# Performance work log

Hardware: AMD Instinct MI355X
Metric: run time of the kernel (lower is better)

## Reference

```python
import jax, jax.numpy as jnp
import numpy as np

B, T, D_ENC, D_DEC, D_ATT = 64, 4096, 512, 512, 256


def setup_inputs() -> dict:
    keys = jax.random.split(jax.random.key(0), 8)
    h_enc = jax.random.normal(keys[0], (B, T, D_ENC), dtype=jnp.float32)
    h_dec = jax.random.normal(keys[1], (B, 1, D_DEC), dtype=jnp.float32)
    mask = jax.random.randint(keys[2], (B, T), 0, 2).astype(bool)
    s = 0.02
    Wq_w = jax.random.normal(keys[3], (D_ATT, D_DEC), dtype=jnp.float32) * s
    Wq_b = jnp.zeros((D_ATT,), dtype=jnp.float32)
    Wk_w = jax.random.normal(keys[4], (D_ATT, D_ENC), dtype=jnp.float32) * s
    Wk_b = jnp.zeros((D_ATT,), dtype=jnp.float32)
    v_w = jax.random.normal(keys[5], (1, D_ATT), dtype=jnp.float32) * s
    return {"h_enc": h_enc, "h_dec": h_dec, "Wq_w": Wq_w, "Wq_b": Wq_b,
            "Wk_w": Wk_w, "Wk_b": Wk_b, "v_w": v_w, "mask": mask}


def reference(h_enc, h_dec, Wq_w, Wq_b, Wk_w, Wk_b, v_w, mask):
    # q: [B,1,d_att], k: [B,T,d_att]
    q = jnp.einsum('bqe,ae->bqa', h_dec, Wq_w) + Wq_b
    k = jnp.einsum('bte,ae->bta', h_enc, Wk_w) + Wk_b
    # additive (Bahdanau) score: v^T tanh(q + k) -> [B,T]
    scores = jnp.einsum('bta,a->bt', jnp.tanh(q + k), v_w[0])
    scores = jnp.where(mask, scores, jnp.float32(-1e9))
    w = jax.nn.softmax(scores, axis=1)          # [B,T]
    ctx = jnp.einsum('bt,bte->be', w, h_enc)    # [B,d_enc]
    return ctx, w
```

## Files before the change

### kernel.cpp

```cpp
#include <hip/hip_runtime.h>
#include <math.h>

#define B    64
#define T    4096
#define DENC 512
#define DDEC 512
#define DATT 256

typedef __attribute__((ext_vector_type(8))) short          short8;
typedef __attribute__((ext_vector_type(8))) unsigned short ushort8v;
typedef __attribute__((ext_vector_type(4))) float          f32x4;

__device__ __forceinline__ unsigned short f2bf(float f) {
    union { float f; unsigned u; } v; v.f = f;
    return (unsigned short)((v.u + 0x7fffu + ((v.u >> 16) & 1u)) >> 16);
}

__device__ __forceinline__ unsigned pk2bf(float a, float b) {
    unsigned ua = __float_as_uint(a) + 0x8000u;
    unsigned ub = __float_as_uint(b) + 0x8000u;
    return __builtin_amdgcn_perm(ub, ua, 0x07060302u);
}

__device__ __forceinline__ float bf2f(unsigned short u) {
    return __uint_as_float((unsigned)u << 16);
}

__device__ __forceinline__ float tanh_fast(float x) {
    float e = __expf(2.0f * x);
    return 1.0f - 2.0f / (e + 1.0f);
}

__global__ __launch_bounds__(256) void k_wkconv(const float* __restrict__ Wk_w,
                                                unsigned short* __restrict__ WkB) {
    int i = (blockIdx.x * 256 + threadIdx.x) * 4;
    float4 v = *(const float4*)(Wk_w + i);
    ushort4 o;
    o.x = f2bf(v.x); o.y = f2bf(v.y); o.z = f2bf(v.z); o.w = f2bf(v.w);
    *(ushort4*)(WkB + i) = o;
}

__global__ __launch_bounds__(256) void k_qproj(const float* __restrict__ h_dec,
                                               const float* __restrict__ Wq_w,
                                               const float* __restrict__ Wq_b,
                                               const float* __restrict__ Wk_b,
                                               float* __restrict__ qq) {
    __shared__ float sh[DDEC];
    const int b = blockIdx.x;
    const int tid = threadIdx.x;
    ((float2*)sh)[tid] = ((const float2*)(h_dec + (size_t)b * DDEC))[tid];
    __syncthreads();
    const int a = tid;
    const float4* wr  = (const float4*)(Wq_w + (size_t)a * DDEC);
    const float4* shv = (const float4*)sh;
    float acc = 0.f;
#pragma unroll 4
    for (int i = 0; i < DDEC / 4; ++i) {
        float4 wv = wr[i];
        float4 hv = shv[i];
        acc += wv.x * hv.x + wv.y * hv.y + wv.z * hv.z + wv.w * hv.w;
    }
    qq[b * DATT + a] = acc + Wq_b[a] + Wk_b[a];
}

#define BM 128
#define BK 32

__global__ __launch_bounds__(256, 2) void k_score(const float* __restrict__ h_enc,
                                                  const unsigned short* __restrict__ WkB,
                                                  const float* __restrict__ qq,
                                                  const float* __restrict__ v_w,
                                                  const int* __restrict__ mask,
                                                  unsigned short* __restrict__ hB,
                                                  float* __restrict__ scores) {
    __shared__ short As[BM * BK];
    __shared__ short Bs[DATT * BK];
    __shared__ float sp[2][BM];

    const int tc   = blockIdx.x;
    const int b    = blockIdx.y;
    const int tid  = threadIdx.x;
    const int wv   = tid >> 6;
    const int lane = tid & 63;
    const int ln15 = lane & 15;
    const int qd   = lane >> 4;
    const int wv_t = wv >> 1;
    const int wv_a = wv & 1;
    const int t0   = tc * BM;

    f32x4 acc[4][8];
#pragma unroll
    for (int i = 0; i < 4; ++i)
#pragma unroll
        for (int j = 0; j < 8; ++j) acc[i][j] = (f32x4){0.f, 0.f, 0.f, 0.f};

    const float* Abase = h_enc + ((size_t)b * T + t0) * DENC;
    unsigned short* hBbase = hB + ((size_t)b * T + t0) * DENC;

    for (int k0 = 0; k0 < DENC; k0 += BK) {
#pragma unroll
        for (int it = 0; it < 4; ++it) {
            int idx = (wv * 4 + it) * 64 + lane;
            int r   = idx >> 2;
            int cc  = (idx & 3) ^ ((r >> 1) & 3);
            const unsigned short* gp = WkB + (size_t)r * DENC + k0 + cc * 8;
            short* lp = &Bs[(wv * 4 + it) * 64 * 8];
            __builtin_amdgcn_global_load_lds(
                (const __attribute__((address_space(1))) unsigned int*)gp,
                (__attribute__((address_space(3))) unsigned int*)lp, 16, 0, 0);
        }
#pragma unroll
        for (int it = 0; it < 2; ++it) {
            int idx = it * 256 + tid;
            int r   = idx >> 2;
            int cc  = (idx & 3) ^ ((r >> 1) & 3);
            const float* gp = Abase + (size_t)r * DENC + k0 + cc * 8;
            float4 v0 = *(const float4*)gp;
            float4 v1 = *(const float4*)(gp + 4);
            uint4 pk;
            pk.x = pk2bf(v0.x, v0.y);
            pk.y = pk2bf(v0.z, v0.w);
            pk.z = pk2bf(v1.x, v1.y);
            pk.w = pk2bf(v1.z, v1.w);
            *(uint4*)&As[idx * 8] = pk;
            *(uint4*)(hBbase + (size_t)r * DENC + k0 + cc * 8) = pk;
        }
        __syncthreads();

        short8 af[4], bfr[8];
#pragma unroll
        for (int ti = 0; ti < 4; ++ti) {
            int r = wv_t * 64 + ti * 16 + ln15;
            int s = qd ^ ((r >> 1) & 3);
            af[ti] = *(const short8*)&As[r * 32 + s * 8];
        }
#pragma unroll
        for (int tj = 0; tj < 8; ++tj) {
            int r = wv_a * 128 + tj * 16 + ln15;
            int s = qd ^ ((r >> 1) & 3);
            bfr[tj] = *(const short8*)&Bs[r * 32 + s * 8];
        }
#pragma unroll
        for (int ti = 0; ti < 4; ++ti)
#pragma unroll
            for (int tj = 0; tj < 8; ++tj)
                acc[ti][tj] = __builtin_amdgcn_mfma_f32_16x16x32_bf16(
                    af[ti], bfr[tj], acc[ti][tj], 0, 0, 0);
        __syncthreads();
    }

    float qr[8], vr[8];
#pragma unroll
    for (int tj = 0; tj < 8; ++tj) {
        int a = wv_a * 128 + tj * 16 + ln15;
        qr[tj] = qq[b * DATT + a];
        vr[tj] = v_w[a];
    }
#pragma unroll
    for (int ti = 0; ti < 4; ++ti) {
#pragma unroll
        for (int rg = 0; rg < 4; ++rg) {
            float s = 0.f;
#pragma unroll
            for (int tj = 0; tj < 8; ++tj)
                s += vr[tj] * tanh_fast(qr[tj] + acc[ti][tj][rg]);
            s += __shfl_xor(s, 1, 64);
            s += __shfl_xor(s, 2, 64);
            s += __shfl_xor(s, 4, 64);
            s += __shfl_xor(s, 8, 64);
            if (ln15 == 0)
                sp[wv_a][wv_t * 64 + ti * 16 + qd * 4 + rg] = s;
        }
    }
    __syncthreads();
    if (tid < BM) {
        int t = t0 + tid;
        float s = sp[0][tid] + sp[1][tid];
        bool m = mask[(size_t)b * T + t] != 0;
        scores[(size_t)b * T + t] = m ? s : -1e9f;
    }
}

__global__ __launch_bounds__(256) void k_softmax(float* __restrict__ w) {
    const int b = blockIdx.x;
    const int tid = threadIdx.x;
    const int wid = tid >> 6, lane = tid & 63;
    float* row = w + (size_t)b * T;
    __shared__ float red[4];
    __shared__ float bmax_s, bsum_s;

    float x[T / 256];
#pragma unroll
    for (int i = 0; i < T / 256; ++i) x[i] = row[tid + i * 256];

    float lmax = -INFINITY;
#pragma unroll
    for (int i = 0; i < T / 256; ++i) lmax = fmaxf(lmax, x[i]);
#pragma unroll
    for (int off = 32; off >= 1; off >>= 1) lmax = fmaxf(lmax, __shfl_xor(lmax, off, 64));
    if (lane == 0) red[wid] = lmax;
    __syncthreads();
    if (tid == 0) bmax_s = fmaxf(fmaxf(red[0], red[1]), fmaxf(red[2], red[3]));
    __syncthreads();
    const float bmax = bmax_s;

    float lsum = 0.f;
#pragma unroll
    for (int i = 0; i < T / 256; ++i) { x[i] = __expf(x[i] - bmax); lsum += x[i]; }
#pragma unroll
    for (int off = 32; off >= 1; off >>= 1) lsum += __shfl_xor(lsum, off, 64);
    if (lane == 0) red[wid] = lsum;
    __syncthreads();
    if (tid == 0) bsum_s = red[0] + red[1] + red[2] + red[3];
    __syncthreads();
    const float inv = 1.f / bsum_s;
#pragma unroll
    for (int i = 0; i < T / 256; ++i) row[tid + i * 256] = x[i] * inv;
}

#define TCH 512
__global__ __launch_bounds__(256) void k_ctx(const unsigned short* __restrict__ hB,
                                             const float* __restrict__ w,
                                             float* __restrict__ ctx) {
    const int b   = blockIdx.y;
    const int t0  = blockIdx.x * TCH;
    const int tid = threadIdx.x;
    const int lane = tid & 63, wv = tid >> 6;
    const int e8 = lane * 8;
    __shared__ float ws[TCH];
    __shared__ float red[3][DENC];

    ((float2*)ws)[tid] = ((const float2*)(w + (size_t)b * T + t0))[tid];
    __syncthreads();

    const unsigned short* hp = hB + ((size_t)(b * T + t0 + wv)) * DENC + e8;
    float a[8];
#pragma unroll
    for (int j = 0; j < 8; ++j) a[j] = 0.f;

#pragma unroll 4
    for (int t = wv; t < TCH; t += 4) {
        float wt = ws[t];
        ushort8v hv = *(const ushort8v*)hp;
        hp += (size_t)4 * DENC;
#pragma unroll
        for (int j = 0; j < 8; ++j)
            a[j] = fmaf(wt, bf2f((unsigned short)hv[j]), a[j]);
    }

    if (wv > 0) {
#pragma unroll
        for (int j = 0; j < 8; ++j) red[wv - 1][e8 + j] = a[j];
    }
    __syncthreads();
    if (wv == 0) {
#pragma unroll
        for (int j = 0; j < 8; ++j) {
            float s = a[j] + red[0][e8 + j] + red[1][e8 + j] + red[2][e8 + j];
            atomicAdd(&ctx[b * DENC + e8 + j], s);
        }
    }
}

extern "C" void kernel_launch(void* const* d_in, const int* in_sizes, int n_in,
                              void* d_out, int out_size, void* d_ws, size_t ws_size,
                              hipStream_t stream) {
    const float* h_enc = (const float*)d_in[0];
    const float* h_dec = (const float*)d_in[1];
    const float* Wq_w  = (const float*)d_in[2];
    const float* Wq_b  = (const float*)d_in[3];
    const float* Wk_w  = (const float*)d_in[4];
    const float* Wk_b  = (const float*)d_in[5];
    const float* v_w   = (const float*)d_in[6];
    const int*   mask  = (const int*)d_in[7];

    float* out = (float*)d_out;
    float* ctx = out;
    float* wts = out + B * DENC;

    float*          qq  = (float*)d_ws;
    unsigned short* WkB = (unsigned short*)((char*)d_ws + (64 << 10));
    unsigned short* hB  = (unsigned short*)((char*)d_ws + (1 << 20));

    hipMemsetAsync(ctx, 0, (size_t)B * DENC * sizeof(float), stream);

    k_wkconv<<<DATT * DENC / 4 / 256, 256, 0, stream>>>(Wk_w, WkB);
    k_qproj<<<B, 256, 0, stream>>>(h_dec, Wq_w, Wq_b, Wk_b, qq);
    k_score<<<dim3(T / BM, B), 256, 0, stream>>>(h_enc, WkB, qq, v_w, mask, hB, wts);
    k_softmax<<<B, 256, 0, stream>>>(wts);
    k_ctx<<<dim3(T / TCH, B), 256, 0, stream>>>(hB, wts, ctx);
}
```

Before: 856.3 us.

## Fuse softmax and context into score kernel with flash-style partial combine

The score kernel now computes a per-chunk max, sum of exponentials and partial context right after scoring, reading the fp32 h_enc tile again while it is likely still in cache. This removes the bf16 copy of h_enc (a large write plus a later reread), the separate softmax and context kernels, and the atomic adds. A small combine kernel rescales the partials and a final kernel normalizes the weights. The cost is a second fp32 pass over each 128-row tile inside the fused kernel and extra workspace for partials.

Result: faster. 804.5 us (-6.0%).

```diff
diff --git a/kernel.cpp b/kernel.cpp
--- a/kernel.cpp
+++ b/kernel.cpp
@@ -7,9 +7,12 @@
 #define DDEC 512
 #define DATT 256
 
-typedef __attribute__((ext_vector_type(8))) short          short8;
-typedef __attribute__((ext_vector_type(8))) unsigned short ushort8v;
-typedef __attribute__((ext_vector_type(4))) float          f32x4;
+#define BM   128
+#define BK   32
+#define NCH  (T / BM)
+
+typedef __attribute__((ext_vector_type(8))) short short8;
+typedef __attribute__((ext_vector_type(4))) float f32x4;
 
 __device__ __forceinline__ unsigned short f2bf(float f) {
     union { float f; unsigned u; } v; v.f = f;
@@ -20,10 +23,6 @@
     unsigned ua = __float_as_uint(a) + 0x8000u;
     unsigned ub = __float_as_uint(b) + 0x8000u;
     return __builtin_amdgcn_perm(ub, ua, 0x07060302u);
-}
-
-__device__ __forceinline__ float bf2f(unsigned short u) {
-    return __uint_as_float((unsigned)u << 16);
 }
 
 __device__ __forceinline__ float tanh_fast(float x) {
@@ -63,19 +62,20 @@
     qq[b * DATT + a] = acc + Wq_b[a] + Wk_b[a];
 }
 
-#define BM 128
-#define BK 32
-
-__global__ __launch_bounds__(256, 2) void k_score(const float* __restrict__ h_enc,
+__global__ __launch_bounds__(256, 2) void k_fused(const float* __restrict__ h_enc,
                                                   const unsigned short* __restrict__ WkB,
                                                   const float* __restrict__ qq,
                                                   const float* __restrict__ v_w,
                                                   const int* __restrict__ mask,
-                                                  unsigned short* __restrict__ hB,
-                                                  float* __restrict__ scores) {
+                                                  float* __restrict__ scores,
+                                                  float* __restrict__ part_m,
+                                                  float* __restrict__ part_l,
+                                                  float* __restrict__ part_ctx) {
     __shared__ short As[BM * BK];
     __shared__ short Bs[DATT * BK];
     __shared__ float sp[2][BM];
+    __shared__ float ps[BM];
+    __shared__ float red_a[4], red_b[4];
 
     const int tc   = blockIdx.x;
     const int b    = blockIdx.y;
@@ -95,7 +95,6 @@
         for (int j = 0; j < 8; ++j) acc[i][j] = (f32x4){0.f, 0.f, 0.f, 0.f};
 
     const float* Abase = h_enc + ((size_t)b * T + t0) * DENC;
-    unsigned short* hBbase = hB + ((size_t)b * T + t0) * DENC;
 
     for (int k0 = 0; k0 < DENC; k0 += BK) {
 #pragma unroll
@@ -123,7 +122,6 @@
             pk.z = pk2bf(v1.x, v1.y);
             pk.w = pk2bf(v1.z, v1.w);
             *(uint4*)&As[idx * 8] = pk;
-            *(uint4*)(hBbase + (size_t)r * DENC + k0 + cc * 8) = pk;
         }
         __syncthreads();
 
@@ -173,93 +171,94 @@
         }
     }
     __syncthreads();
+
     if (tid < BM) {
         int t = t0 + tid;
         float s = sp[0][tid] + sp[1][tid];
-        bool m = mask[(size_t)b * T + t] != 0;
-        scores[(size_t)b * T + t] = m ? s : -1e9f;
-    }
-}
-
-__global__ __launch_bounds__(256) void k_softmax(float* __restrict__ w) {
+        bool mk = mask[(size_t)b * T + t] != 0;
+        s = mk ? s : -1e9f;
+        scores[(size_t)b * T + t] = s;
+        ps[tid] = s;
+    }
+    __syncthreads();
+
+    float mv = (tid < BM) ? ps[tid] : -INFINITY;
+#pragma unroll
+    for (int off = 32; off >= 1; off >>= 1) mv = fmaxf(mv, __shfl_xor(mv, off, 64));
+    if (lane == 0) red_a[wv] = mv;
+    __syncthreads();
+    const float M = fmaxf(fmaxf(red_a[0], red_a[1]), fmaxf(red_a[2], red_a[3]));
+
+    float p = 0.f;
+    if (tid < BM) { p = __expf(ps[tid] - M); ps[tid] = p; }
+    float ls = p;
+#pragma unroll
+    for (int off = 32; off >= 1; off >>= 1) ls += __shfl_xor(ls, off, 64);
+    if (lane == 0) red_b[wv] = ls;
+    __syncthreads();
+    if (tid == 0) {
+        part_m[b * NCH + tc] = M;
+        part_l[b * NCH + tc] = red_b[0] + red_b[1] + red_b[2] + red_b[3];
+    }
+
+    const float2* hp = (const float2*)(Abase) + tid;
+    float ax = 0.f, ay = 0.f;
+#pragma unroll 8
+    for (int t = 0; t < BM; ++t) {
+        float pt = ps[t];
+        float2 hv = hp[(size_t)t * (DENC / 2)];
+        ax = fmaf(pt, hv.x, ax);
+        ay = fmaf(pt, hv.y, ay);
+    }
+    float2* pc = (float2*)(part_ctx + ((size_t)(b * NCH + tc)) * DENC) + tid;
+    *pc = make_float2(ax, ay);
+}
+
+__global__ __launch_bounds__(256) void k_combine(const float* __restrict__ part_m,
+                                                 const float* __restrict__ part_l,
+                                                 const float* __restrict__ part_ctx,
+                                                 float* __restrict__ ctx,
+                                                 float2* __restrict__ ml) {
     const int b = blockIdx.x;
     const int tid = threadIdx.x;
-    const int wid = tid >> 6, lane = tid & 63;
-    float* row = w + (size_t)b * T;
-    __shared__ float red[4];
-    __shared__ float bmax_s, bsum_s;
-
-    float x[T / 256];
-#pragma unroll
-    for (int i = 0; i < T / 256; ++i) x[i] = row[tid + i * 256];
-
-    float lmax = -INFINITY;
-#pragma unroll
-    for (int i = 0; i < T / 256; ++i) lmax = fmaxf(lmax, x[i]);
-#pragma unroll
-    for (int off = 32; off >= 1; off >>= 1) lmax = fmaxf(lmax, __shfl_xor(lmax, off, 64));
-    if (lane == 0) red[wid] = lmax;
-    __syncthreads();
-    if (tid == 0) bmax_s = fmaxf(fmaxf(red[0], red[1]), fmaxf(red[2], red[3]));
-    __syncthreads();
-    const float bmax = bmax_s;
-
-    float lsum = 0.f;
-#pragma unroll
-    for (int i = 0; i < T / 256; ++i) { x[i] = __expf(x[i] - bmax); lsum += x[i]; }
-#pragma unroll
-    for (int off = 32; off >= 1; off >>= 1) lsum += __shfl_xor(lsum, off, 64);
-    if (lane == 0) red[wid] = lsum;
-    __syncthreads();
-    if (tid == 0) bsum_s = red[0] + red[1] + red[2] + red[3];
-    __syncthreads();
-    const float inv = 1.f / bsum_s;
-#pragma unroll
-    for (int i = 0; i < T / 256; ++i) row[tid + i * 256] = x[i] * inv;
-}
-
-#define TCH 512
-__global__ __launch_bounds__(256) void k_ctx(const unsigned short* __restrict__ hB,
-                                             const float* __restrict__ w,
-                                             float* __restrict__ ctx) {
-    const int b   = blockIdx.y;
-    const int t0  = blockIdx.x * TCH;
-    const int tid = threadIdx.x;
-    const int lane = tid & 63, wv = tid >> 6;
-    const int e8 = lane * 8;
-    __shared__ float ws[TCH];
-    __shared__ float red[3][DENC];
-
-    ((float2*)ws)[tid] = ((const float2*)(w + (size_t)b * T + t0))[tid];
-    __syncthreads();
-
-    const unsigned short* hp = hB + ((size_t)(b * T + t0 + wv)) * DENC + e8;
-    float a[8];
-#pragma unroll
-    for (int j = 0; j < 8; ++j) a[j] = 0.f;
-
+    __shared__ float sm[NCH], sl[NCH];
+    if (tid < NCH) {
+        sm[tid] = part_m[b * NCH + tid];
+        sl[tid] = part_l[b * NCH + tid];
+    }
+    __syncthreads();
+    float M = -INFINITY;
+#pragma unroll
+    for (int i = 0; i < NCH; ++i) M = fmaxf(M, sm[i]);
+
+    float L = 0.f, ax = 0.f, ay = 0.f;
+    const float2* pc = (const float2*)(part_ctx + (size_t)b * NCH * DENC) + tid;
 #pragma unroll 4
-    for (int t = wv; t < TCH; t += 4) {
-        float wt = ws[t];
-        ushort8v hv = *(const ushort8v*)hp;
-        hp += (size_t)4 * DENC;
-#pragma unroll
-        for (int j = 0; j < 8; ++j)
-            a[j] = fmaf(wt, bf2f((unsigned short)hv[j]), a[j]);
-    }
-
-    if (wv > 0) {
-#pragma unroll
-        for (int j = 0; j < 8; ++j) red[wv - 1][e8 + j] = a[j];
-    }
-    __syncthreads();
-    if (wv == 0) {
-#pragma unroll
-        for (int j = 0; j < 8; ++j) {
-            float s = a[j] + red[0][e8 + j] + red[1][e8 + j] + red[2][e8 + j];
-            atomicAdd(&ctx[b * DENC + e8 + j], s);
-        }
-    }
+    for (int i = 0; i < NCH; ++i) {
+        float sc = __expf(sm[i] - M);
+        L += sl[i] * sc;
+        float2 v = pc[(size_t)i * (DENC / 2)];
+        ax = fmaf(sc, v.x, ax);
+        ay = fmaf(sc, v.y, ay);
+    }
+    float inv = 1.f / L;
+    ((float2*)(ctx + b * DENC))[tid] = make_float2(ax * inv, ay * inv);
+    if (tid == 0) ml[b] = make_float2(M, inv);
+}
+
+__global__ __launch_bounds__(256) void k_w(const float* __restrict__ scores,
+                                           const float2* __restrict__ ml,
+                                           float* __restrict__ w) {
+    const int b = blockIdx.y;
+    float2 m = ml[b];
+    size_t off = (size_t)b * T + blockIdx.x * 1024 + threadIdx.x * 4;
+    float4 s = *(const float4*)(scores + off);
+    float4 o;
+    o.x = __expf(s.x - m.x) * m.y;
+    o.y = __expf(s.y - m.x) * m.y;
+    o.z = __expf(s.z - m.x) * m.y;
+    o.w = __expf(s.w - m.x) * m.y;
+    *(float4*)(w + off) = o;
 }
 
 extern "C" void kernel_launch(void* const* d_in, const int* in_sizes, int n_in,
@@ -278,15 +277,19 @@
     float* ctx = out;
     float* wts = out + B * DENC;
 
-    float*          qq  = (float*)d_ws;
-    unsigned short* WkB = (unsigned short*)((char*)d_ws + (64 << 10));
-    unsigned short* hB  = (unsigned short*)((char*)d_ws + (1 << 20));
-
-    hipMemsetAsync(ctx, 0, (size_t)B * DENC * sizeof(float), stream);
+    char* ws = (char*)d_ws;
+    float*          qq       = (float*)ws;
+    unsigned short* WkB      = (unsigned short*)(ws + (64 << 10));
+    float*          scores   = (float*)(ws + (1 << 20));
+    float*          part_m   = (float*)(ws + (2 << 20));
+    float*          part_l   = (float*)(ws + (2 << 20) + (16 << 10));
+    float2*         ml       = (float2*)(ws + (2 << 20) + (32 << 10));
+    float*          part_ctx = (float*)(ws + (3 << 20));
 
     k_wkconv<<<DATT * DENC / 4 / 256, 256, 0, stream>>>(Wk_w, WkB);
     k_qproj<<<B, 256, 0, stream>>>(h_dec, Wq_w, Wq_b, Wk_b, qq);
-    k_score<<<dim3(T / BM, B), 256, 0, stream>>>(h_enc, WkB, qq, v_w, mask, hB, wts);
-    k_softmax<<<B, 256, 0, stream>>>(wts);
-    k_ctx<<<dim3(T / TCH, B), 256, 0, stream>>>(hB, wts, ctx);
-}
+    k_fused<<<dim3(NCH, B), 256, 0, stream>>>(h_enc, WkB, qq, v_w, mask,
+                                              scores, part_m, part_l, part_ctx);
+    k_combine<<<B, 256, 0, stream>>>(part_m, part_l, part_ctx, ctx, ml);
+    k_w<<<dim3(T / 1024, B), 256, 0, stream>>>(scores, ml, wts);
+}
```
